# Kernel tuning notes

Measured on AMD Instinct MI355X. Metric: run time of the kernel, lower is better.

Reference implementation:

```python
import jax, jax.numpy as jnp
import numpy as np
from jax import lax

VOCAB, EMBED, HIDDEN = 50000, 300, 512
BATCH, SEQ = 64, 512


def setup_inputs() -> dict:
    key = jax.random.key(0)
    ks = jax.random.split(key, 8)
    return {
        "x_indx": jax.random.randint(ks[0], (BATCH, SEQ), 0, VOCAB),
        "embeddings": jax.random.normal(ks[1], (VOCAB, EMBED), dtype=jnp.float32),
        "W_ih": jax.random.normal(ks[2], (4 * HIDDEN, EMBED), dtype=jnp.float32) * 0.02,
        "W_hh": jax.random.normal(ks[3], (4 * HIDDEN, HIDDEN), dtype=jnp.float32) * 0.02,
        "b_ih": jax.random.normal(ks[4], (4 * HIDDEN,), dtype=jnp.float32) * 0.02,
        "b_hh": jax.random.normal(ks[5], (4 * HIDDEN,), dtype=jnp.float32) * 0.02,
        "W_out": jax.random.normal(ks[6], (1, HIDDEN), dtype=jnp.float32) * 0.02,
        "b_out": jax.random.normal(ks[7], (1,), dtype=jnp.float32) * 0.02,
    }


def _lstm_final_hidden(x, W_ih, W_hh, b_ih, b_hh):
    # x: [B, S, E] -> final hidden state h_T: [B, H]
    B = x.shape[0]
    H = W_hh.shape[1]
    # Precompute input projections for all timesteps: [S, B, 4H]
    x_proj = jnp.einsum('bse,ge->sbg', x, W_ih) + b_ih + b_hh

    def step(carry, xp):
        h, c = carry
        gates = xp + h @ W_hh.T  # [B, 4H], PyTorch gate order i,f,g,o
        i, f, g, o = jnp.split(gates, 4, axis=-1)
        i = jax.nn.sigmoid(i)
        f = jax.nn.sigmoid(f)
        g = jnp.tanh(g)
        o = jax.nn.sigmoid(o)
        c = f * c + i * g
        h = o * jnp.tanh(c)
        return (h, c), None

    h0 = jnp.zeros((B, H), dtype=x.dtype)
    c0 = jnp.zeros((B, H), dtype=x.dtype)
    (hT, cT), _ = lax.scan(step, (h0, c0), x_proj)
    return hT


def reference(x_indx, embeddings, W_ih, W_hh, b_ih, b_hh, W_out, b_out):
    # Frozen embedding lookup: [B, S, E]
    x = embeddings[x_indx]
    hT = _lstm_final_hidden(x, W_ih, W_hh, b_ih, b_hh)  # [B, H]
    return hT @ W_out.T + b_out  # [B, 1]
```

## Files before the change

### kernel.cpp

```cpp
#include <hip/hip_runtime.h>
#include <hip/hip_bf16.h>

typedef short  bf16x8 __attribute__((ext_vector_type(8)));
typedef float  f32x4  __attribute__((ext_vector_type(4)));
typedef int    i32x4  __attribute__((ext_vector_type(4)));

#define BB 64
#define SS 512
#define EE 300
#define HH 512

#define XT_OFF     ((size_t)0)
#define XT_BYTES   ((size_t)SS*10*4*1024)
#define SLOT_OFF   (XT_OFF + XT_BYTES)
#define SLOT_BYTES ((size_t)2*4*16*128*16)
#define HT_OFF     (SLOT_OFF + SLOT_BYTES)
#define HT_BYTES   ((size_t)BB*HH*4)

__device__ __forceinline__ unsigned short f2bf(float x) {
  union { float f; unsigned u; } v; v.f = x;
  unsigned r = v.u + 0x7fffu + ((v.u >> 16) & 1u);
  return (unsigned short)(r >> 16);
}
__device__ __forceinline__ float sigm(float x) { return 1.f / (1.f + __expf(-x)); }
__device__ __forceinline__ float tanh_fast(float x) { return 1.f - 2.f / (__expf(2.f * x) + 1.f); }

__device__ __forceinline__ void ld16_cc(i32x4* dst, const void* p) {
  asm volatile("global_load_dwordx4 %0, %1, off sc0 sc1"
               : "=v"(*dst) : "v"(p) : "memory");
}
__device__ __forceinline__ void st16_cc(void* p, i32x4 v) {
  asm volatile("global_store_dwordx4 %0, %1, off sc0 sc1"
               :: "v"(p), "v"(v) : "memory");
}

__global__ void gather_cast_kernel(const int* __restrict__ idx,
                                   const float* __restrict__ emb,
                                   unsigned short* __restrict__ xt) {
  __shared__ unsigned short lds_x[16 * 320];
  const int t     = blockIdx.x >> 2;
  const int mtile = blockIdx.x & 3;
  const int tid   = threadIdx.x;

  const int c2 = tid >> 4;
  const int e0 = tid & 15;
  const int b  = mtile * 16 + c2;
  const int vocab = idx[b * SS + t];
  const float* src = emb + (size_t)vocab * EE;
  for (int e = e0; e < 320; e += 16)
    lds_x[c2 * 320 + e] = (e < EE) ? f2bf(src[e]) : (unsigned short)0;
  __syncthreads();

  unsigned short* outb = xt + (((size_t)t * 10) * 4 + mtile) * 512;
  #pragma unroll
  for (int rr = 0; rr < 3; ++rr) {
    int O = rr * 4096 + tid * 16;
    if (O < 10240) {
      int ks = O >> 10;
      int inblk = O & 1023;
      int c  = inblk >> 6;
      int kg = (inblk >> 4) & 3;
      bf16x8 v = *(const bf16x8*)&lds_x[c * 320 + ks * 32 + kg * 8];
      *(bf16x8*)((char*)outb + (size_t)ks * 4096 + inblk) = v;
    }
  }
}

__launch_bounds__(512, 2)
__global__ void lstm_kernel(const unsigned short* __restrict__ xt,
                            char* __restrict__ slots,
                            float* __restrict__ hT,
                            const float* __restrict__ Wih,
                            const float* __restrict__ Whh,
                            const float* __restrict__ bih,
                            const float* __restrict__ bhh) {
  __shared__ __attribute__((aligned(16))) char hstage[2][16 * 1280];

  const int p   = blockIdx.x;
  const int sg  = p & 3;
  const int uw  = p >> 2;
  const int tid = threadIdx.x;
  const int l   = tid & 63;
  const int w   = tid >> 6;
  const int c   = l & 15;
  const int kg  = l >> 4;
  const int U0  = 32 * uw + 4 * w;

  const int Grow = ((c >> 2) << 9) + U0 + (c & 3);
  const float* wih_row = Wih + (size_t)Grow * EE;
  const float* whh_row = Whh + (size_t)Grow * HH;

  bf16x8 Bx[10], Bh[16];
  #pragma unroll
  for (int ks = 0; ks < 10; ++ks) {
    int k0 = 32 * ks + 8 * kg;
    bf16x8 vb;
    #pragma unroll
    for (int j = 0; j < 8; ++j) {
      int k = k0 + j;
      vb[j] = (short)((k < EE) ? f2bf(wih_row[k]) : (unsigned short)0);
    }
    Bx[ks] = vb;
  }
  #pragma unroll
  for (int kt = 0; kt < 16; ++kt) {
    int k0 = 32 * kt + 8 * kg;
    bf16x8 vb;
    #pragma unroll
    for (int j = 0; j < 8; ++j) vb[j] = (short)f2bf(whh_row[k0 + j]);
    Bh[kt] = vb;
  }
  const float bsum = bih[Grow] + bhh[Grow];

  const unsigned short* xbase = xt + sg * 512 + c * 32 + kg * 8;

  const int uq_t = tid & 127;
  const int s0_t = tid >> 7;
  const int lwb  = (uq_t >> 3) * 1280 + ((uq_t >> 1) & 3) * 16 + (uq_t & 1) * 8
                 + s0_t * 80;
  const size_t sg_off = (size_t)sg * 32768;
  const char* rbase = slots + sg_off + (size_t)tid * 16;
  const int lr = c * 80 + kg * 16;
  char* const wbase = slots + sg_off + (size_t)(8 * uw + w) * 16;

  f32x4 cst = {0.f, 0.f, 0.f, 0.f};

  for (int it = 0; it < SS; ++it) {
    const char* rp = rbase + (size_t)(it & 1) * 131072;
    i32x4 d0, d1, d2, d3;
    ld16_cc(&d0, rp);
    ld16_cc(&d1, rp + 8192);
    ld16_cc(&d2, rp + 16384);
    ld16_cc(&d3, rp + 24576);

    f32x4 ax0 = {0.f, 0.f, 0.f, 0.f};
    f32x4 ax1 = {0.f, 0.f, 0.f, 0.f};
    const unsigned short* xq = xbase + (size_t)it * 20480;
    #pragma unroll
    for (int ks = 0; ks < 10; ks += 2) {
      bf16x8 a0 = *(const bf16x8*)(xq + ks * 2048);
      bf16x8 a1 = *(const bf16x8*)(xq + (ks + 1) * 2048);
      ax0 = __builtin_amdgcn_mfma_f32_16x16x32_bf16(a0, Bx[ks],     ax0, 0, 0, 0);
      ax1 = __builtin_amdgcn_mfma_f32_16x16x32_bf16(a1, Bx[ks + 1], ax1, 0, 0, 0);
    }
    __builtin_amdgcn_sched_barrier(0);

    asm volatile("s_waitcnt vmcnt(0)" ::: "memory");
    while (!((d0[2] == it) & (d1[2] == it) & (d2[2] == it) & (d3[2] == it))) {
      __builtin_amdgcn_s_sleep(1);
      ld16_cc(&d0, rp);
      ld16_cc(&d1, rp + 8192);
      ld16_cc(&d2, rp + 16384);
      ld16_cc(&d3, rp + 24576);
      asm volatile("s_waitcnt vmcnt(0)" ::: "memory");
    }

    char* hs = hstage[it & 1];
    { int* q = (int*)(hs + lwb);        q[0] = d0[0]; q[1] = d0[1]; }
    { int* q = (int*)(hs + lwb + 320);  q[0] = d1[0]; q[1] = d1[1]; }
    { int* q = (int*)(hs + lwb + 640);  q[0] = d2[0]; q[1] = d2[1]; }
    { int* q = (int*)(hs + lwb + 960);  q[0] = d3[0]; q[1] = d3[1]; }
    __syncthreads();

    f32x4 ah0 = {0.f, 0.f, 0.f, 0.f};
    f32x4 ah1 = {0.f, 0.f, 0.f, 0.f};
    #pragma unroll
    for (int kt = 0; kt < 16; kt += 2) {
      bf16x8 a0 = *(const bf16x8*)(hs + kt * 1280 + lr);
      bf16x8 a1 = *(const bf16x8*)(hs + (kt + 1) * 1280 + lr);
      ah0 = __builtin_amdgcn_mfma_f32_16x16x32_bf16(a0, Bh[kt],     ah0, 0, 0, 0);
      ah1 = __builtin_amdgcn_mfma_f32_16x16x32_bf16(a1, Bh[kt + 1], ah1, 0, 0, 0);
    }
    f32x4 acc = (ax0 + ax1) + (ah0 + ah1);

    char* wp = wbase + (size_t)((it + 1) & 1) * 131072;
    #pragma unroll
    for (int r = 0; r < 4; ++r) {
      float v  = acc[r] + bsum;
      float vf = __shfl_xor(v, 4, 64);
      float vg = __shfl_xor(v, 8, 64);
      float vo = __shfl_xor(v, 12, 64);
      float ig = sigm(v);
      float fg = sigm(vf);
      float gt = tanh_fast(vg);
      float og = sigm(vo);
      cst[r] = fg * cst[r] + ig * gt;
      float h = og * tanh_fast(cst[r]);

      if (it != SS - 1) {
        int hv  = (int)f2bf(h);
        int o1  = __shfl_xor(hv, 1, 64);
        int pk  = (hv & 0xffff) | (o1 << 16);
        int pk2 = __shfl_xor(pk, 2, 64);
        if (c == 0) {
          i32x4 val; val[0] = pk; val[1] = pk2; val[2] = it + 1; val[3] = 0;
          st16_cc(wp + (4 * kg + r) * 2048, val);
        }
      } else if (c < 4) {
        hT[(size_t)(16 * sg + 4 * kg + r) * HH + U0 + c] = h;
      }
    }
  }
}

__global__ void outproj_kernel(const float* __restrict__ hT,
                               const float* __restrict__ Wout,
                               const float* __restrict__ bout,
                               float* __restrict__ y) {
  int b = blockIdx.x;
  int t = threadIdx.x;
  float s = 0.f;
  for (int j = t; j < HH; j += 64) s += hT[b * HH + j] * Wout[j];
  #pragma unroll
  for (int off = 32; off > 0; off >>= 1) s += __shfl_down(s, off, 64);
  if (t == 0) y[b] = s + bout[0];
}

extern "C" void kernel_launch(void* const* d_in, const int* in_sizes, int n_in,
                              void* d_out, int out_size, void* d_ws, size_t ws_size,
                              hipStream_t stream) {
  const int*   idx  = (const int*)d_in[0];
  const float* emb  = (const float*)d_in[1];
  const float* Wih  = (const float*)d_in[2];
  const float* Whh  = (const float*)d_in[3];
  const float* bih  = (const float*)d_in[4];
  const float* bhh  = (const float*)d_in[5];
  const float* Wout = (const float*)d_in[6];
  const float* bout = (const float*)d_in[7];
  float* y = (float*)d_out;

  char* ws = (char*)d_ws;
  unsigned short* xt = (unsigned short*)(ws + XT_OFF);
  char* slots        = ws + SLOT_OFF;
  float* hT          = (float*)(ws + HT_OFF);

  hipMemsetAsync(slots, 0, SLOT_BYTES, stream);

  gather_cast_kernel<<<SS * 4, 256, 0, stream>>>(idx, emb, xt);
  lstm_kernel<<<64, 512, 0, stream>>>(xt, slots, hT, Wih, Whh, bih, bhh);
  outproj_kernel<<<BB, 64, 0, stream>>>(hT, Wout, bout, y);
}
```

Measured before the change: 2.420 ms.

## Restructure LSTM into single-wave blocks reading h directly from global slots

Replaces 64 blocks of 8 waves (with an LDS restage and __syncthreads each step) by 256 single-wave blocks. Each wave owns 8 hidden units for one 16-row batch tile, holding both weight sets in registers. Each wave loads its MFMA A-operands for h straight from a 4-plane global slot buffer, so the LDS staging and block barrier go away. The input-projection MFMAs overlap the coherent slot loads. In exchange there are many more flag-checking loads per wave, higher register pressure from the doubled weight arrays, and more blocks spin-waiting on each other, which needs all 256 blocks co-resident to avoid deadlock.

```diff
diff --git a/kernel.cpp b/kernel.cpp
--- a/kernel.cpp
+++ b/kernel.cpp
@@ -10,12 +10,13 @@
 #define EE 300
 #define HH 512
 
-#define XT_OFF     ((size_t)0)
-#define XT_BYTES   ((size_t)SS*10*4*1024)
-#define SLOT_OFF   (XT_OFF + XT_BYTES)
-#define SLOT_BYTES ((size_t)2*4*16*128*16)
-#define HT_OFF     (SLOT_OFF + SLOT_BYTES)
-#define HT_BYTES   ((size_t)BB*HH*4)
+#define XT_OFF      ((size_t)0)
+#define XT_BYTES    ((size_t)SS*10*4*1024)
+#define SLOT_OFF    (XT_OFF + XT_BYTES)
+#define PLANE_B     ((size_t)64*128*16)
+#define SLOT_BYTES  ((size_t)4*PLANE_B)
+#define HT_OFF      (SLOT_OFF + SLOT_BYTES)
+#define HT_BYTES    ((size_t)BB*HH*4)
 
 __device__ __forceinline__ unsigned short f2bf(float x) {
   union { float f; unsigned u; } v; v.f = x;
@@ -24,15 +25,6 @@
 }
 __device__ __forceinline__ float sigm(float x) { return 1.f / (1.f + __expf(-x)); }
 __device__ __forceinline__ float tanh_fast(float x) { return 1.f - 2.f / (__expf(2.f * x) + 1.f); }
-
-__device__ __forceinline__ void ld16_cc(i32x4* dst, const void* p) {
-  asm volatile("global_load_dwordx4 %0, %1, off sc0 sc1"
-               : "=v"(*dst) : "v"(p) : "memory");
-}
-__device__ __forceinline__ void st16_cc(void* p, i32x4 v) {
-  asm volatile("global_store_dwordx4 %0, %1, off sc0 sc1"
-               :: "v"(p), "v"(v) : "memory");
-}
 
 __global__ void gather_cast_kernel(const int* __restrict__ idx,
                                    const float* __restrict__ emb,
@@ -66,7 +58,7 @@
   }
 }
 
-__launch_bounds__(512, 2)
+__launch_bounds__(64, 1)
 __global__ void lstm_kernel(const unsigned short* __restrict__ xt,
                             char* __restrict__ slots,
                             float* __restrict__ hT,
@@ -74,130 +66,156 @@
                             const float* __restrict__ Whh,
                             const float* __restrict__ bih,
                             const float* __restrict__ bhh) {
-  __shared__ __attribute__((aligned(16))) char hstage[2][16 * 1280];
-
-  const int p   = blockIdx.x;
-  const int sg  = p & 3;
-  const int uw  = p >> 2;
-  const int tid = threadIdx.x;
-  const int l   = tid & 63;
-  const int w   = tid >> 6;
-  const int c   = l & 15;
-  const int kg  = l >> 4;
-  const int U0  = 32 * uw + 4 * w;
-
-  const int Grow = ((c >> 2) << 9) + U0 + (c & 3);
-  const float* wih_row = Wih + (size_t)Grow * EE;
-  const float* whh_row = Whh + (size_t)Grow * HH;
-
-  bf16x8 Bx[10], Bh[16];
-  #pragma unroll
-  for (int ks = 0; ks < 10; ++ks) {
-    int k0 = 32 * ks + 8 * kg;
-    bf16x8 vb;
-    #pragma unroll
-    for (int j = 0; j < 8; ++j) {
-      int k = k0 + j;
-      vb[j] = (short)((k < EE) ? f2bf(wih_row[k]) : (unsigned short)0);
-    }
-    Bx[ks] = vb;
+  const int p  = blockIdx.x >> 2;
+  const int mt = blockIdx.x & 3;
+  const int l  = threadIdx.x;
+  const int c  = l & 15;
+  const int kg = l >> 4;
+
+  const int G0 = ((c >> 2) << 9) + (p << 3) + (c & 3);
+  const int G1 = G0 + 4;
+  bf16x8 Bx0[10], Bx1[10], Bh0[16], Bh1[16];
+  {
+    const float* w0 = Wih + (size_t)G0 * EE;
+    const float* w1 = Wih + (size_t)G1 * EE;
+    #pragma unroll
+    for (int ks = 0; ks < 10; ++ks) {
+      int k0 = 32 * ks + 8 * kg;
+      bf16x8 v0, v1;
+      #pragma unroll
+      for (int j = 0; j < 8; ++j) {
+        int k = k0 + j;
+        v0[j] = (short)((k < EE) ? f2bf(w0[k]) : (unsigned short)0);
+        v1[j] = (short)((k < EE) ? f2bf(w1[k]) : (unsigned short)0);
+      }
+      Bx0[ks] = v0; Bx1[ks] = v1;
+    }
+    const float* h0 = Whh + (size_t)G0 * HH;
+    const float* h1 = Whh + (size_t)G1 * HH;
+    #pragma unroll
+    for (int ks = 0; ks < 16; ++ks) {
+      int k0 = 32 * ks + 8 * kg;
+      bf16x8 v0, v1;
+      #pragma unroll
+      for (int j = 0; j < 8; ++j) {
+        v0[j] = (short)f2bf(h0[k0 + j]);
+        v1[j] = (short)f2bf(h1[k0 + j]);
+      }
+      Bh0[ks] = v0; Bh1[ks] = v1;
+    }
   }
-  #pragma unroll
-  for (int kt = 0; kt < 16; ++kt) {
-    int k0 = 32 * kt + 8 * kg;
-    bf16x8 vb;
-    #pragma unroll
-    for (int j = 0; j < 8; ++j) vb[j] = (short)f2bf(whh_row[k0 + j]);
-    Bh[kt] = vb;
-  }
-  const float bsum = bih[Grow] + bhh[Grow];
-
-  const unsigned short* xbase = xt + sg * 512 + c * 32 + kg * 8;
-
-  const int uq_t = tid & 127;
-  const int s0_t = tid >> 7;
-  const int lwb  = (uq_t >> 3) * 1280 + ((uq_t >> 1) & 3) * 16 + (uq_t & 1) * 8
-                 + s0_t * 80;
-  const size_t sg_off = (size_t)sg * 32768;
-  const char* rbase = slots + sg_off + (size_t)tid * 16;
-  const int lr = c * 80 + kg * 16;
-  char* const wbase = slots + sg_off + (size_t)(8 * uw + w) * 16;
-
-  f32x4 cst = {0.f, 0.f, 0.f, 0.f};
+  const float bc0 = bih[G0] + bhh[G0];
+  const float bc1 = bih[G1] + bhh[G1];
+
+  const unsigned short* xbase = xt + mt * 512 + c * 32 + kg * 8;
+  const int rb = (16 * mt + c) * 2048 + kg * 32;
+  const int wb = (16 * mt) * 2048 + 2 * p * 16;
+  float cst0[4] = {0.f, 0.f, 0.f, 0.f};
+  float cst1[4] = {0.f, 0.f, 0.f, 0.f};
 
   for (int it = 0; it < SS; ++it) {
-    const char* rp = rbase + (size_t)(it & 1) * 131072;
-    i32x4 d0, d1, d2, d3;
-    ld16_cc(&d0, rp);
-    ld16_cc(&d1, rp + 8192);
-    ld16_cc(&d2, rp + 16384);
-    ld16_cc(&d3, rp + 24576);
-
-    f32x4 ax0 = {0.f, 0.f, 0.f, 0.f};
-    f32x4 ax1 = {0.f, 0.f, 0.f, 0.f};
     const unsigned short* xq = xbase + (size_t)it * 20480;
-    #pragma unroll
-    for (int ks = 0; ks < 10; ks += 2) {
-      bf16x8 a0 = *(const bf16x8*)(xq + ks * 2048);
-      bf16x8 a1 = *(const bf16x8*)(xq + (ks + 1) * 2048);
-      ax0 = __builtin_amdgcn_mfma_f32_16x16x32_bf16(a0, Bx[ks],     ax0, 0, 0, 0);
-      ax1 = __builtin_amdgcn_mfma_f32_16x16x32_bf16(a1, Bx[ks + 1], ax1, 0, 0, 0);
-    }
+    bf16x8 xa[10];
+    #pragma unroll
+    for (int ks = 0; ks < 10; ++ks)
+      asm volatile("global_load_dwordx4 %0, %1, off"
+                   : "=v"(xa[ks]) : "v"(xq + ks * 2048) : "memory");
+
+    const char* rp = slots + (size_t)(it & 3) * PLANE_B + rb;
+    i32x4 sA[16], sB[16];
+    #pragma unroll
+    for (int ks = 0; ks < 16; ++ks) {
+      asm volatile("global_load_dwordx4 %0, %1, off sc0 sc1"
+                   : "=v"(sA[ks]) : "v"(rp + ks * 128) : "memory");
+      asm volatile("global_load_dwordx4 %0, %1, off sc0 sc1"
+                   : "=v"(sB[ks]) : "v"(rp + ks * 128 + 16) : "memory");
+    }
+
+    asm volatile("s_waitcnt vmcnt(32)" ::: "memory");
     __builtin_amdgcn_sched_barrier(0);
+    f32x4 a0 = {bc0, bc0, bc0, bc0};
+    f32x4 a1 = {bc1, bc1, bc1, bc1};
+    #pragma unroll
+    for (int ks = 0; ks < 10; ++ks) {
+      a0 = __builtin_amdgcn_mfma_f32_16x16x32_bf16(xa[ks], Bx0[ks], a0, 0, 0, 0);
+      a1 = __builtin_amdgcn_mfma_f32_16x16x32_bf16(xa[ks], Bx1[ks], a1, 0, 0, 0);
+    }
 
     asm volatile("s_waitcnt vmcnt(0)" ::: "memory");
-    while (!((d0[2] == it) & (d1[2] == it) & (d2[2] == it) & (d3[2] == it))) {
+    __builtin_amdgcn_sched_barrier(0);
+    for (;;) {
+      int ok = 1;
+      #pragma unroll
+      for (int ks = 0; ks < 16; ++ks)
+        ok &= (sA[ks][2] == it) & (sB[ks][2] == it);
+      if (__all(ok)) break;
       __builtin_amdgcn_s_sleep(1);
-      ld16_cc(&d0, rp);
-      ld16_cc(&d1, rp + 8192);
-      ld16_cc(&d2, rp + 16384);
-      ld16_cc(&d3, rp + 24576);
+      #pragma unroll
+      for (int ks = 0; ks < 16; ++ks) {
+        asm volatile("global_load_dwordx4 %0, %1, off sc0 sc1"
+                     : "=v"(sA[ks]) : "v"(rp + ks * 128) : "memory");
+        asm volatile("global_load_dwordx4 %0, %1, off sc0 sc1"
+                     : "=v"(sB[ks]) : "v"(rp + ks * 128 + 16) : "memory");
+      }
       asm volatile("s_waitcnt vmcnt(0)" ::: "memory");
-    }
-
-    char* hs = hstage[it & 1];
-    { int* q = (int*)(hs + lwb);        q[0] = d0[0]; q[1] = d0[1]; }
-    { int* q = (int*)(hs + lwb + 320);  q[0] = d1[0]; q[1] = d1[1]; }
-    { int* q = (int*)(hs + lwb + 640);  q[0] = d2[0]; q[1] = d2[1]; }
-    { int* q = (int*)(hs + lwb + 960);  q[0] = d3[0]; q[1] = d3[1]; }
-    __syncthreads();
-
-    f32x4 ah0 = {0.f, 0.f, 0.f, 0.f};
-    f32x4 ah1 = {0.f, 0.f, 0.f, 0.f};
-    #pragma unroll
-    for (int kt = 0; kt < 16; kt += 2) {
-      bf16x8 a0 = *(const bf16x8*)(hs + kt * 1280 + lr);
-      bf16x8 a1 = *(const bf16x8*)(hs + (kt + 1) * 1280 + lr);
-      ah0 = __builtin_amdgcn_mfma_f32_16x16x32_bf16(a0, Bh[kt],     ah0, 0, 0, 0);
-      ah1 = __builtin_amdgcn_mfma_f32_16x16x32_bf16(a1, Bh[kt + 1], ah1, 0, 0, 0);
-    }
-    f32x4 acc = (ax0 + ax1) + (ah0 + ah1);
-
-    char* wp = wbase + (size_t)((it + 1) & 1) * 131072;
+      __builtin_amdgcn_sched_barrier(0);
+    }
+
+    #pragma unroll
+    for (int ks = 0; ks < 16; ++ks) {
+      i32x4 t;
+      t[0] = sA[ks][0]; t[1] = sA[ks][1]; t[2] = sB[ks][0]; t[3] = sB[ks][1];
+      bf16x8 a = __builtin_bit_cast(bf16x8, t);
+      a0 = __builtin_amdgcn_mfma_f32_16x16x32_bf16(a, Bh0[ks], a0, 0, 0, 0);
+      a1 = __builtin_amdgcn_mfma_f32_16x16x32_bf16(a, Bh1[ks], a1, 0, 0, 0);
+    }
+
+    char* wp = slots + (size_t)((it + 1) & 3) * PLANE_B + wb;
     #pragma unroll
     for (int r = 0; r < 4; ++r) {
-      float v  = acc[r] + bsum;
-      float vf = __shfl_xor(v, 4, 64);
-      float vg = __shfl_xor(v, 8, 64);
-      float vo = __shfl_xor(v, 12, 64);
-      float ig = sigm(v);
-      float fg = sigm(vf);
-      float gt = tanh_fast(vg);
-      float og = sigm(vo);
-      cst[r] = fg * cst[r] + ig * gt;
-      float h = og * tanh_fast(cst[r]);
-
-      if (it != SS - 1) {
-        int hv  = (int)f2bf(h);
-        int o1  = __shfl_xor(hv, 1, 64);
-        int pk  = (hv & 0xffff) | (o1 << 16);
-        int pk2 = __shfl_xor(pk, 2, 64);
-        if (c == 0) {
-          i32x4 val; val[0] = pk; val[1] = pk2; val[2] = it + 1; val[3] = 0;
-          st16_cc(wp + (4 * kg + r) * 2048, val);
+      {
+        float v  = a0[r];
+        float vf = __shfl_xor(v, 4, 64);
+        float vg = __shfl_xor(v, 8, 64);
+        float vo = __shfl_xor(v, 12, 64);
+        float ig = sigm(v), fg = sigm(vf), og = sigm(vo), gt = tanh_fast(vg);
+        cst0[r] = fg * cst0[r] + ig * gt;
+        float h = og * tanh_fast(cst0[r]);
+        if (it != SS - 1) {
+          int hv  = (int)f2bf(h);
+          int o1  = __shfl_xor(hv, 1, 64);
+          int pk  = (hv & 0xffff) | (o1 << 16);
+          int pk2 = __shfl_xor(pk, 2, 64);
+          if (c == 0) {
+            i32x4 val; val[0] = pk; val[1] = pk2; val[2] = it + 1; val[3] = 0;
+            asm volatile("global_store_dwordx4 %0, %1, off sc0 sc1"
+                         :: "v"(wp + (4 * kg + r) * 2048), "v"(val) : "memory");
+          }
+        } else if (c < 4) {
+          hT[(size_t)(16 * mt + 4 * kg + r) * HH + (p << 3) + c] = h;
         }
-      } else if (c < 4) {
-        hT[(size_t)(16 * sg + 4 * kg + r) * HH + U0 + c] = h;
+      }
+      {
+        float v  = a1[r];
+        float vf = __shfl_xor(v, 4, 64);
+        float vg = __shfl_xor(v, 8, 64);
+        float vo = __shfl_xor(v, 12, 64);
+        float ig = sigm(v), fg = sigm(vf), og = sigm(vo), gt = tanh_fast(vg);
+        cst1[r] = fg * cst1[r] + ig * gt;
+        float h = og * tanh_fast(cst1[r]);
+        if (it != SS - 1) {
+          int hv  = (int)f2bf(h);
+          int o1  = __shfl_xor(hv, 1, 64);
+          int pk  = (hv & 0xffff) | (o1 << 16);
+          int pk2 = __shfl_xor(pk, 2, 64);
+          if (c == 0) {
+            i32x4 val; val[0] = pk; val[1] = pk2; val[2] = it + 1; val[3] = 0;
+            asm volatile("global_store_dwordx4 %0, %1, off sc0 sc1"
+                         :: "v"(wp + (4 * kg + r) * 2048 + 16), "v"(val) : "memory");
+          }
+        } else if (c < 4) {
+          hT[(size_t)(16 * mt + 4 * kg + r) * HH + (p << 3) + 4 + c] = h;
+        }
       }
     }
   }
@@ -237,6 +255,6 @@
   hipMemsetAsync(slots, 0, SLOT_BYTES, stream);
 
   gather_cast_kernel<<<SS * 4, 256, 0, stream>>>(idx, emb, xt);
-  lstm_kernel<<<64, 512, 0, stream>>>(xt, slots, hT, Wih, Whh, bih, bhh);
+  lstm_kernel<<<256, 64, 0, stream>>>(xt, slots, hT, Wih, Whh, bih, bhh);
   outproj_kernel<<<BB, 64, 0, stream>>>(hT, Wout, bout, y);
 }
```

After: 3.707 ms. 1.53x slower.
